# Performance work log

Measured on AMD Instinct MI355X. Metric: run time of the kernel, lower is better.

The kernel has to match this reference:

```python
import jax, jax.numpy as jnp
import numpy as np

EPS = 1e-5

def setup_inputs() -> dict:
    key = jax.random.key(0)
    ks = jax.random.split(key, 4)
    B, N, L, D, H = 1, 32, 512, 256, 8
    msa = jax.random.normal(ks[0], (B, N, L, D), dtype=jnp.float32)
    pair_bias = jax.random.normal(ks[1], (B, L, L, H), dtype=jnp.float32)
    # parameters (fan-in scaled like nn.Linear init magnitude)
    w_qkv = jax.random.normal(ks[2], (D, 3 * D), dtype=jnp.float32) / np.sqrt(D)
    b_qkv = jnp.zeros((3 * D,), dtype=jnp.float32)
    w_proj = jax.random.normal(ks[3], (D, D), dtype=jnp.float32) / np.sqrt(D)
    b_proj = jnp.zeros((D,), dtype=jnp.float32)
    ln_w = jnp.ones((D,), dtype=jnp.float32)
    ln_b = jnp.zeros((D,), dtype=jnp.float32)
    return {"msa": msa, "pair_bias": pair_bias, "ln_w": ln_w, "ln_b": ln_b,
            "w_qkv": w_qkv, "b_qkv": b_qkv, "w_proj": w_proj, "b_proj": b_proj}

def reference(msa, pair_bias, ln_w, ln_b, w_qkv, b_qkv, w_proj, b_proj):
    B, N, L, D = msa.shape
    H = pair_bias.shape[-1]
    hd = D // H
    # LayerNorm over last dim (biased variance, eps=1e-5, as in nn.LayerNorm)
    mu = jnp.mean(msa, axis=-1, keepdims=True)
    var = jnp.mean(jnp.square(msa - mu), axis=-1, keepdims=True)
    m = (msa - mu) * jax.lax.rsqrt(var + EPS) * ln_w + ln_b
    # fused QKV projection; output dim 3*D splits as (3, H, hd)
    qkv = jnp.einsum('bnld,de->bnle', m, w_qkv) + b_qkv  # (B,N,L,3D)
    qkv = qkv.reshape(B, N, L, 3, H, hd)
    q = qkv[:, :, :, 0]  # (B,N,L,H,hd)
    k = qkv[:, :, :, 1]
    v = qkv[:, :, :, 2]
    scale = 1.0 / np.sqrt(hd).astype(np.float32)
    attn = jnp.einsum('bnqhd,bnkhd->bnhqk', q, k) * scale  # (B,N,H,L,L)
    # pair bias (B,L,L,H) -> (B,1,H,L,L), broadcast over the N_seq rows
    attn = attn + jnp.transpose(pair_bias, (0, 3, 1, 2))[:, None]
    attn = jax.nn.softmax(attn, axis=-1)
    out = jnp.einsum('bnhqk,bnkhd->bnqhd', attn, v).reshape(B, N, L, D)
    out = jnp.einsum('bnld,de->bnle', out, w_proj) + b_proj
    return msa + out
```

## Files before the change

kernel.cpp:

```cpp
#include <hip/hip_runtime.h>
#include <hip/hip_bf16.h>

typedef __attribute__((ext_vector_type(8))) short short8;
typedef __attribute__((ext_vector_type(4))) float f32x4;

#define LOG2E 1.4426950408889634f
#define QSCALE 0.25505403955318165f

static __device__ __forceinline__ unsigned short f2bf(float f){
  union { float f; unsigned u; } v; v.f = f;
  unsigned r = v.u + 0x7fffu + ((v.u >> 16) & 1u);
  return (unsigned short)(r >> 16);
}
static __device__ __forceinline__ float bf2f(unsigned short s){
  union { unsigned u; float f; } v; v.u = ((unsigned)s) << 16; return v.f;
}
static __device__ __forceinline__ unsigned cvt_pk_bf16(float lo, float hi){
  unsigned r;
  asm("v_cvt_pk_bf16_f32 %0, %1, %2" : "=v"(r) : "v"(lo), "v"(hi));
  return r;
}
static __device__ __forceinline__ void gload_lds16(const void* g, void* l){
  __builtin_amdgcn_global_load_lds((const __attribute__((address_space(1))) unsigned*)g,
                                   (__attribute__((address_space(3))) unsigned*)l, 16, 0, 0);
}

__global__ __launch_bounds__(256) void k_prep(
    const float* __restrict__ w_qkv, const float* __restrict__ w_proj,
    const float* __restrict__ pb, const float* __restrict__ msa,
    const float* __restrict__ ln_w, const float* __restrict__ ln_b,
    unsigned short* __restrict__ wqkvT, unsigned short* __restrict__ wprojT,
    unsigned short* __restrict__ bt, unsigned short* __restrict__ m_bf){
  __shared__ float tile[64][65];
  int b = blockIdx.x;
  int tid = threadIdx.x;
  if (b < 64){
    const float* in;
    unsigned short* outp;
    int C, tc;
    if (b < 48){ in = w_qkv; outp = wqkvT; C = 768; tc = 12; b -= 0; }
    else       { in = w_proj; outp = wprojT; C = 256; tc = 4;  b -= 48; }
    int r0 = (b / tc) * 64, c0 = (b % tc) * 64;
#pragma unroll
    for (int it = 0; it < 16; it++){
      int idx = tid + it*256, ri = idx >> 6, ci = idx & 63;
      tile[ri][ci] = in[(size_t)(r0+ri)*C + c0+ci];
    }
    __syncthreads();
#pragma unroll
    for (int it = 0; it < 16; it++){
      int idx = tid + it*256, co = idx >> 6, ro = idx & 63;
      outp[(size_t)(c0+co)*256 + r0+ro] = f2bf(tile[ro][co]);
    }
  } else if (b < 1088){
    int bid = b - 64;
    int q = bid >> 1;
    int k = ((bid & 1) << 8) + tid;
    int kc = k >> 6, tl = (k >> 4) & 3, gg = (k >> 2) & 3, r = k & 3;
    int kp = kc*64 + gg*16 + tl*4 + r;
    const float* src = pb + ((size_t)q * 512 + k) * 8;
    float4 a = *(const float4*)src;
    float4 c = *(const float4*)(src + 4);
    float hv[8] = {a.x, a.y, a.z, a.w, c.x, c.y, c.z, c.w};
#pragma unroll
    for (int hh = 0; hh < 8; hh++)
      bt[((size_t)hh * 512 + q) * 512 + kp] = f2bf(hv[hh] * LOG2E);
  } else {
    int wave = tid >> 6, lane = tid & 63;
    int row = (b - 1088) * 4 + wave;
    const float* xr = msa + (size_t)row * 256 + lane * 4;
    float4 v = *(const float4*)xr;
    float s  = v.x + v.y + v.z + v.w;
    float sq = v.x*v.x + v.y*v.y + v.z*v.z + v.w*v.w;
#pragma unroll
    for (int off = 1; off < 64; off <<= 1){ s += __shfl_xor(s, off); sq += __shfl_xor(sq, off); }
    float mu = s * (1.0f/256.0f);
    float var = sq * (1.0f/256.0f) - mu*mu;
    float rs = rsqrtf(var + 1e-5f);
    float4 wv = *(const float4*)(ln_w + lane*4);
    float4 bv = *(const float4*)(ln_b + lane*4);
    uint2 o;
    o.x = cvt_pk_bf16((v.x-mu)*rs*wv.x + bv.x, (v.y-mu)*rs*wv.y + bv.y);
    o.y = cvt_pk_bf16((v.z-mu)*rs*wv.z + bv.z, (v.w-mu)*rs*wv.w + bv.w);
    *(uint2*)(m_bf + (size_t)row * 256 + lane * 4) = o;
  }
}

__global__ __launch_bounds__(256) void k_gemm_qkv(const unsigned short* __restrict__ A,
    const unsigned short* __restrict__ Bt, const float* __restrict__ bias,
    unsigned short* __restrict__ Qb, unsigned short* __restrict__ Kb, unsigned short* __restrict__ Vb){
  __shared__ unsigned short As[128*64];
  __shared__ unsigned short Bs[128*64];
  int bid0 = blockIdx.x;
  int bid = (bid0 & 7) * 96 + (bid0 >> 3);
  int bn = bid % 6, bm = bid / 6;
  int m0 = bm * 128, e0 = bn * 128;
  int t = threadIdx.x, lane = t & 63, w = t >> 6;
  int wm = w >> 1, wn = w & 1;
  int g = lane >> 4, mm = lane & 15;
  f32x4 acc[4][4] = {};
  for (int k0 = 0; k0 < 256; k0 += 64){
    __syncthreads();
#pragma unroll
    for (int it = 0; it < 4; it++){
      int task = t + it * 256;
      int row = task >> 3, ch = task & 7;
      gload_lds16(A  + (size_t)(m0+row)*256 + k0 + ch*8, &As[task*8]);
      gload_lds16(Bt + (size_t)(e0+row)*256 + k0 + ch*8, &Bs[task*8]);
    }
    __syncthreads();
#pragma unroll
    for (int kst = 0; kst < 2; kst++){
      short8 a[4], bb[4];
#pragma unroll
      for (int i = 0; i < 4; i++)
        a[i]  = *(short8*)(&As[(wm*64 + i*16 + mm)*64 + kst*32 + g*8]);
#pragma unroll
      for (int j = 0; j < 4; j++)
        bb[j] = *(short8*)(&Bs[(wn*64 + j*16 + mm)*64 + kst*32 + g*8]);
#pragma unroll
      for (int i = 0; i < 4; i++)
#pragma unroll
        for (int j = 0; j < 4; j++)
          acc[i][j] = __builtin_amdgcn_mfma_f32_16x16x32_bf16(a[i], bb[j], acc[i][j], 0, 0, 0);
    }
  }
#pragma unroll
  for (int i = 0; i < 4; i++)
#pragma unroll
    for (int j = 0; j < 4; j++){
      int col = e0 + wn*64 + j*16 + mm;
      float bc = bias[col];
      int sidx = col >> 8, hh = (col >> 5) & 7, d = col & 31;
      unsigned short* dst = (sidx == 0) ? Qb : ((sidx == 1) ? Kb : Vb);
      float sc = (sidx == 0) ? QSCALE : 1.0f;
#pragma unroll
      for (int r = 0; r < 4; r++){
        int gm = m0 + wm*64 + i*16 + 4*g + r;
        int nn = gm >> 9, l = gm & 511;
        dst[(((size_t)nn*8 + hh)*512 + l)*32 + d] = f2bf((acc[i][j][r] + bc) * sc);
      }
    }
}

__global__ __launch_bounds__(512) void k_attn(const unsigned short* __restrict__ Qb,
    const unsigned short* __restrict__ Kb, const unsigned short* __restrict__ Vb,
    const unsigned short* __restrict__ bt, unsigned short* __restrict__ Ob){
  __shared__ unsigned short Ks[512*40];
  __shared__ unsigned short Vs[32*520];
  int bid = blockIdx.x;
  int h = bid & 7;
  int n = (bid >> 3) & 31;
  int qq = bid >> 8;
  int nh = n*8 + h;
  int t = threadIdx.x;
  int lane = t & 63, wv = t >> 6;
  int g = lane >> 4, q16 = lane & 15;
  const unsigned short* kbase = Kb + (size_t)nh * 16384;
  const unsigned short* vbase = Vb + (size_t)nh * 16384;
  const unsigned short* qbase = Qb + (size_t)nh * 16384;
  {
    int row = t;
    const uint4* ksrc = (const uint4*)(kbase + row * 32);
#pragma unroll
    for (int j = 0; j < 4; j++) *(uint4*)(&Ks[row*40 + j*8]) = ksrc[j];
    int prow = (row & ~12) | ((row & 4) << 1) | ((row & 8) >> 1);
    const uint* vsrc = (const uint*)(vbase + row * 32);
    uint vv[16];
#pragma unroll
    for (int j = 0; j < 16; j++) vv[j] = vsrc[j];
#pragma unroll
    for (int j = 0; j < 16; j++){
      Vs[(2*j)*520 + prow]   = (unsigned short)(vv[j] & 0xffffu);
      Vs[(2*j+1)*520 + prow] = (unsigned short)(vv[j] >> 16);
    }
  }
  __syncthreads();
  {
    int qb = qq*128 + wv*16;
    int qg = qb + q16;
    short8 qf = *(const short8*)(qbase + (size_t)qg * 32 + g * 8);
    const unsigned short* bq = bt + ((size_t)(h*512 + qg))*512 + g*16;
    f32x4 ls4 = {0.0f, 0.0f, 0.0f, 0.0f};
    f32x4 acc[2] = {{0,0,0,0},{0,0,0,0}};
    f32x4 zf = {0.0f, 0.0f, 0.0f, 0.0f};
    uint4 bn0 = *(const uint4*)(bq);
    uint4 bn1 = *(const uint4*)(bq + 8);
#pragma unroll 2
    for (int kc = 0; kc < 8; kc++){
      union { uint4 w[2]; unsigned short u[16]; } bu;
      bu.w[0] = bn0; bu.w[1] = bn1;
      if (kc < 7){
        bn0 = *(const uint4*)(bq + (kc+1)*64);
        bn1 = *(const uint4*)(bq + (kc+1)*64 + 8);
      }
      f32x4 s[4];
      __builtin_amdgcn_s_setprio(1);
#pragma unroll
      for (int tl = 0; tl < 4; tl++){
        short8 kf = *(short8*)(&Ks[(kc*64 + tl*16 + q16)*40 + g*8]);
        s[tl] = __builtin_amdgcn_mfma_f32_16x16x32_bf16(kf, qf, zf, 0, 0, 0);
      }
      __builtin_amdgcn_s_setprio(0);
#pragma unroll
      for (int tl = 0; tl < 4; tl++){
        f32x4 pz;
#pragma unroll
        for (int r = 0; r < 4; r++){
          float e = __builtin_amdgcn_exp2f(s[tl][r] + bf2f(bu.u[tl*4+r]));
          pz[r] = e;
          ls4[r] += e;
        }
        s[tl] = pz;
      }
#pragma unroll
      for (int cl = 0; cl < 2; cl++){
        unsigned a0 = cvt_pk_bf16(s[2*cl][0],   s[2*cl][1]);
        unsigned a1 = cvt_pk_bf16(s[2*cl][2],   s[2*cl][3]);
        unsigned b0 = cvt_pk_bf16(s[2*cl+1][0], s[2*cl+1][1]);
        unsigned b1 = cvt_pk_bf16(s[2*cl+1][2], s[2*cl+1][3]);
        asm("v_permlane32_swap_b32 %0, %1" : "+v"(a0), "+v"(b0));
        asm("v_permlane32_swap_b32 %0, %1" : "+v"(a1), "+v"(b1));
        union { unsigned w[4]; short8 pf; } u;
        u.w[0] = a0; u.w[1] = a1; u.w[2] = b0; u.w[3] = b1;
        __builtin_amdgcn_s_setprio(1);
#pragma unroll
        for (int half = 0; half < 2; half++){
          short8 vf = *(short8*)(&Vs[(half*16 + q16)*520 + kc*64 + cl*32 + g*8]);
          acc[half] = __builtin_amdgcn_mfma_f32_16x16x32_bf16(u.pf, vf, acc[half], 0, 0, 0);
        }
        __builtin_amdgcn_s_setprio(0);
      }
    }
    float ls = (ls4[0] + ls4[1]) + (ls4[2] + ls4[3]);
    ls += __shfl_xor(ls, 16);
    ls += __shfl_xor(ls, 32);
    float linv[4];
#pragma unroll
    for (int r = 0; r < 4; r++) linv[r] = 1.0f / __shfl(ls, 4*g + r);
#pragma unroll
    for (int half = 0; half < 2; half++)
#pragma unroll
      for (int r = 0; r < 4; r++){
        int ql = qb + 4*g + r;
        Ob[((size_t)n*512 + ql)*256 + h*32 + half*16 + q16] = f2bf(acc[half][r] * linv[r]);
      }
  }
}

__global__ __launch_bounds__(256) void k_gemm_proj(const unsigned short* __restrict__ A,
    const unsigned short* __restrict__ Bt, const float* __restrict__ bias,
    const float* __restrict__ msa, float* __restrict__ out){
  __shared__ unsigned short As[64*64];
  __shared__ unsigned short Bs[128*64];
  int bid0 = blockIdx.x;
  int bid = (bid0 & 7) * 64 + (bid0 >> 3);
  int bn = bid & 1, bm = bid >> 1;
  int m0 = bm * 64, e0 = bn * 128;
  int t = threadIdx.x, lane = t & 63, w = t >> 6;
  int g = lane >> 4, mm = lane & 15;
  f32x4 acc[4][2] = {};
  for (int k0 = 0; k0 < 256; k0 += 64){
    __syncthreads();
#pragma unroll
    for (int it = 0; it < 2; it++){
      int task = t + it * 256;
      gload_lds16(A + (size_t)(m0+(task>>3))*256 + k0 + (task&7)*8, &As[task*8]);
    }
#pragma unroll
    for (int it = 0; it < 4; it++){
      int task = t + it * 256;
      gload_lds16(Bt + (size_t)(e0+(task>>3))*256 + k0 + (task&7)*8, &Bs[task*8]);
    }
    __syncthreads();
#pragma unroll
    for (int kst = 0; kst < 2; kst++){
      short8 a[4], bb[2];
#pragma unroll
      for (int i = 0; i < 4; i++)
        a[i] = *(short8*)(&As[(i*16 + mm)*64 + kst*32 + g*8]);
#pragma unroll
      for (int j = 0; j < 2; j++)
        bb[j] = *(short8*)(&Bs[(w*32 + j*16 + mm)*64 + kst*32 + g*8]);
#pragma unroll
      for (int i = 0; i < 4; i++)
#pragma unroll
        for (int j = 0; j < 2; j++)
          acc[i][j] = __builtin_amdgcn_mfma_f32_16x16x32_bf16(a[i], bb[j], acc[i][j], 0, 0, 0);
    }
  }
#pragma unroll
  for (int i = 0; i < 4; i++)
#pragma unroll
    for (int j = 0; j < 2; j++){
      int col = e0 + w*32 + j*16 + mm;
      float bc = bias[col];
#pragma unroll
      for (int r = 0; r < 4; r++){
        int gm = m0 + i*16 + 4*g + r;
        size_t idx = (size_t)gm * 256 + col;
        out[idx] = acc[i][j][r] + bc + msa[idx];
      }
    }
}

extern "C" void kernel_launch(void* const* d_in, const int* in_sizes, int n_in,
                              void* d_out, int out_size, void* d_ws, size_t ws_size,
                              hipStream_t stream){
  const float* msa    = (const float*)d_in[0];
  const float* pb     = (const float*)d_in[1];
  const float* ln_w   = (const float*)d_in[2];
  const float* ln_b   = (const float*)d_in[3];
  const float* w_qkv  = (const float*)d_in[4];
  const float* b_qkv  = (const float*)d_in[5];
  const float* w_proj = (const float*)d_in[6];
  const float* b_proj = (const float*)d_in[7];

  unsigned short* ws     = (unsigned short*)d_ws;
  unsigned short* m_bf   = ws;
  unsigned short* wqkvT  = m_bf   + 4194304;
  unsigned short* wprojT = wqkvT  + 196608;
  unsigned short* Qb     = wprojT + 65536;
  unsigned short* Kb     = Qb     + 4194304;
  unsigned short* Vb     = Kb     + 4194304;
  unsigned short* Ob     = Vb     + 4194304;
  unsigned short* bt     = Ob     + 4194304;
  float* out = (float*)d_out;

  k_prep<<<5184, 256, 0, stream>>>(w_qkv, w_proj, pb, msa, ln_w, ln_b, wqkvT, wprojT, bt, m_bf);
  k_gemm_qkv<<<768, 256, 0, stream>>>(m_bf, wqkvT, b_qkv, Qb, Kb, Vb);
  k_attn<<<1024, 512, 0, stream>>>(Qb, Kb, Vb, bt, Ob);
  k_gemm_proj<<<512, 256, 0, stream>>>(Ob, wprojT, b_proj, msa, out);
}
```

Baseline: 66.66 us.

## Process two query tiles per attention block to reuse staged K/V

Each attention block now handles 256 query rows (two 16-row tiles per wave) instead of 128, halving the grid to 512 blocks. The K and V tiles staged in LDS, including the transposed V copy, are reused across twice as many queries, which halves the global K/V loading and staging work. Two independent MFMA chains per wave also add instruction-level parallelism. In exchange, register pressure roughly doubles and there are fewer blocks, which may reduce occupancy and the ability to hide latency across the 256 CUs.

After: 65.69 us. About the same (-1.4%).

```diff
diff --git a/kernel.cpp b/kernel.cpp
--- a/kernel.cpp
+++ b/kernel.cpp
@@ -151,7 +151,7 @@
   int bid = blockIdx.x;
   int h = bid & 7;
   int n = (bid >> 3) & 31;
-  int qq = bid >> 8;
+  int qh = bid >> 8;
   int nh = n*8 + h;
   int t = threadIdx.x;
   int lane = t & 63, wv = t >> 6;
@@ -177,73 +177,94 @@
   }
   __syncthreads();
   {
-    int qb = qq*128 + wv*16;
-    int qg = qb + q16;
-    short8 qf = *(const short8*)(qbase + (size_t)qg * 32 + g * 8);
-    const unsigned short* bq = bt + ((size_t)(h*512 + qg))*512 + g*16;
-    f32x4 ls4 = {0.0f, 0.0f, 0.0f, 0.0f};
-    f32x4 acc[2] = {{0,0,0,0},{0,0,0,0}};
+    int qb = qh*256 + wv*16;
+    int qgA = qb + q16, qgB = qgA + 128;
+    short8 qfA = *(const short8*)(qbase + (size_t)qgA * 32 + g * 8);
+    short8 qfB = *(const short8*)(qbase + (size_t)qgB * 32 + g * 8);
+    const unsigned short* bqA = bt + ((size_t)(h*512 + qgA))*512 + g*16;
+    const unsigned short* bqB = bt + ((size_t)(h*512 + qgB))*512 + g*16;
+    f32x4 lsA = {0.0f, 0.0f, 0.0f, 0.0f}, lsB = {0.0f, 0.0f, 0.0f, 0.0f};
+    f32x4 accA[2] = {{0,0,0,0},{0,0,0,0}};
+    f32x4 accB[2] = {{0,0,0,0},{0,0,0,0}};
     f32x4 zf = {0.0f, 0.0f, 0.0f, 0.0f};
-    uint4 bn0 = *(const uint4*)(bq);
-    uint4 bn1 = *(const uint4*)(bq + 8);
+    uint4 bnA0 = *(const uint4*)(bqA), bnA1 = *(const uint4*)(bqA + 8);
+    uint4 bnB0 = *(const uint4*)(bqB), bnB1 = *(const uint4*)(bqB + 8);
 #pragma unroll 2
     for (int kc = 0; kc < 8; kc++){
-      union { uint4 w[2]; unsigned short u[16]; } bu;
-      bu.w[0] = bn0; bu.w[1] = bn1;
+      union { uint4 w[2]; unsigned short u[16]; } buA, buB;
+      buA.w[0] = bnA0; buA.w[1] = bnA1;
+      buB.w[0] = bnB0; buB.w[1] = bnB1;
       if (kc < 7){
-        bn0 = *(const uint4*)(bq + (kc+1)*64);
-        bn1 = *(const uint4*)(bq + (kc+1)*64 + 8);
-      }
-      f32x4 s[4];
+        bnA0 = *(const uint4*)(bqA + (kc+1)*64);
+        bnA1 = *(const uint4*)(bqA + (kc+1)*64 + 8);
+        bnB0 = *(const uint4*)(bqB + (kc+1)*64);
+        bnB1 = *(const uint4*)(bqB + (kc+1)*64 + 8);
+      }
+      f32x4 sA[4], sB[4];
       __builtin_amdgcn_s_setprio(1);
 #pragma unroll
       for (int tl = 0; tl < 4; tl++){
         short8 kf = *(short8*)(&Ks[(kc*64 + tl*16 + q16)*40 + g*8]);
-        s[tl] = __builtin_amdgcn_mfma_f32_16x16x32_bf16(kf, qf, zf, 0, 0, 0);
+        sA[tl] = __builtin_amdgcn_mfma_f32_16x16x32_bf16(kf, qfA, zf, 0, 0, 0);
+        sB[tl] = __builtin_amdgcn_mfma_f32_16x16x32_bf16(kf, qfB, zf, 0, 0, 0);
       }
       __builtin_amdgcn_s_setprio(0);
 #pragma unroll
       for (int tl = 0; tl < 4; tl++){
-        f32x4 pz;
 #pragma unroll
         for (int r = 0; r < 4; r++){
-          float e = __builtin_amdgcn_exp2f(s[tl][r] + bf2f(bu.u[tl*4+r]));
-          pz[r] = e;
-          ls4[r] += e;
+          float eA = __builtin_amdgcn_exp2f(sA[tl][r] + bf2f(buA.u[tl*4+r]));
+          sA[tl][r] = eA; lsA[r] += eA;
+          float eB = __builtin_amdgcn_exp2f(sB[tl][r] + bf2f(buB.u[tl*4+r]));
+          sB[tl][r] = eB; lsB[r] += eB;
         }
-        s[tl] = pz;
       }
 #pragma unroll
       for (int cl = 0; cl < 2; cl++){
-        unsigned a0 = cvt_pk_bf16(s[2*cl][0],   s[2*cl][1]);
-        unsigned a1 = cvt_pk_bf16(s[2*cl][2],   s[2*cl][3]);
-        unsigned b0 = cvt_pk_bf16(s[2*cl+1][0], s[2*cl+1][1]);
-        unsigned b1 = cvt_pk_bf16(s[2*cl+1][2], s[2*cl+1][3]);
-        asm("v_permlane32_swap_b32 %0, %1" : "+v"(a0), "+v"(b0));
-        asm("v_permlane32_swap_b32 %0, %1" : "+v"(a1), "+v"(b1));
-        union { unsigned w[4]; short8 pf; } u;
-        u.w[0] = a0; u.w[1] = a1; u.w[2] = b0; u.w[3] = b1;
+        unsigned a0A = cvt_pk_bf16(sA[2*cl][0],   sA[2*cl][1]);
+        unsigned a1A = cvt_pk_bf16(sA[2*cl][2],   sA[2*cl][3]);
+        unsigned b0A = cvt_pk_bf16(sA[2*cl+1][0], sA[2*cl+1][1]);
+        unsigned b1A = cvt_pk_bf16(sA[2*cl+1][2], sA[2*cl+1][3]);
+        asm("v_permlane32_swap_b32 %0, %1" : "+v"(a0A), "+v"(b0A));
+        asm("v_permlane32_swap_b32 %0, %1" : "+v"(a1A), "+v"(b1A));
+        unsigned a0B = cvt_pk_bf16(sB[2*cl][0],   sB[2*cl][1]);
+        unsigned a1B = cvt_pk_bf16(sB[2*cl][2],   sB[2*cl][3]);
+        unsigned b0B = cvt_pk_bf16(sB[2*cl+1][0], sB[2*cl+1][1]);
+        unsigned b1B = cvt_pk_bf16(sB[2*cl+1][2], sB[2*cl+1][3]);
+        asm("v_permlane32_swap_b32 %0, %1" : "+v"(a0B), "+v"(b0B));
+        asm("v_permlane32_swap_b32 %0, %1" : "+v"(a1B), "+v"(b1B));
+        union { unsigned w[4]; short8 pf; } uA, uB;
+        uA.w[0] = a0A; uA.w[1] = a1A; uA.w[2] = b0A; uA.w[3] = b1A;
+        uB.w[0] = a0B; uB.w[1] = a1B; uB.w[2] = b0B; uB.w[3] = b1B;
         __builtin_amdgcn_s_setprio(1);
 #pragma unroll
         for (int half = 0; half < 2; half++){
           short8 vf = *(short8*)(&Vs[(half*16 + q16)*520 + kc*64 + cl*32 + g*8]);
-          acc[half] = __builtin_amdgcn_mfma_f32_16x16x32_bf16(u.pf, vf, acc[half], 0, 0, 0);
+          accA[half] = __builtin_amdgcn_mfma_f32_16x16x32_bf16(uA.pf, vf, accA[half], 0, 0, 0);
+          accB[half] = __builtin_amdgcn_mfma_f32_16x16x32_bf16(uB.pf, vf, accB[half], 0, 0, 0);
         }
         __builtin_amdgcn_s_setprio(0);
       }
     }
-    float ls = (ls4[0] + ls4[1]) + (ls4[2] + ls4[3]);
-    ls += __shfl_xor(ls, 16);
-    ls += __shfl_xor(ls, 32);
-    float linv[4];
-#pragma unroll
-    for (int r = 0; r < 4; r++) linv[r] = 1.0f / __shfl(ls, 4*g + r);
+    float lA = (lsA[0] + lsA[1]) + (lsA[2] + lsA[3]);
+    lA += __shfl_xor(lA, 16);
+    lA += __shfl_xor(lA, 32);
+    float lB = (lsB[0] + lsB[1]) + (lsB[2] + lsB[3]);
+    lB += __shfl_xor(lB, 16);
+    lB += __shfl_xor(lB, 32);
+    float linvA[4], linvB[4];
+#pragma unroll
+    for (int r = 0; r < 4; r++){
+      linvA[r] = 1.0f / __shfl(lA, 4*g + r);
+      linvB[r] = 1.0f / __shfl(lB, 4*g + r);
+    }
 #pragma unroll
     for (int half = 0; half < 2; half++)
 #pragma unroll
       for (int r = 0; r < 4; r++){
         int ql = qb + 4*g + r;
-        Ob[((size_t)n*512 + ql)*256 + h*32 + half*16 + q16] = f2bf(acc[half][r] * linv[r]);
+        Ob[((size_t)n*512 + ql)*256 + h*32 + half*16 + q16] = f2bf(accA[half][r] * linvA[r]);
+        Ob[((size_t)n*512 + ql + 128)*256 + h*32 + half*16 + q16] = f2bf(accB[half][r] * linvB[r]);
       }
   }
 }
@@ -329,6 +350,6 @@
 
   k_prep<<<5184, 256, 0, stream>>>(w_qkv, w_proj, pb, msa, ln_w, ln_b, wqkvT, wprojT, bt, m_bf);
   k_gemm_qkv<<<768, 256, 0, stream>>>(m_bf, wqkvT, b_qkv, Qb, Kb, Vb);
-  k_attn<<<1024, 512, 0, stream>>>(Qb, Kb, Vb, bt, Ob);
+  k_attn<<<512, 512, 0, stream>>>(Qb, Kb, Vb, bt, Ob);
   k_gemm_proj<<<512, 256, 0, stream>>>(Ob, wprojT, b_proj, msa, out);
 }
```

## Stage K/V in two halves to halve attention LDS footprint

Applied to the files above, without the earlier changes.

The attention kernel now stages K and V into shared memory 256 keys at a time instead of all 512, with threads 0-255 loading K and 256-511 loading V. Shared memory per block roughly halves, which could let more blocks reside per CU. The cost is an extra pair of barriers mid-loop plus a serialized reload that is not overlapped with compute. Each thread also does half as much staging work, with a different split of threads between the K and V loads.

Result: slower. 69.77 us (+4.7%).

```diff
diff --git a/kernel.cpp b/kernel.cpp
--- a/kernel.cpp
+++ b/kernel.cpp
@@ -146,8 +146,8 @@
 __global__ __launch_bounds__(512) void k_attn(const unsigned short* __restrict__ Qb,
     const unsigned short* __restrict__ Kb, const unsigned short* __restrict__ Vb,
     const unsigned short* __restrict__ bt, unsigned short* __restrict__ Ob){
-  __shared__ unsigned short Ks[512*40];
-  __shared__ unsigned short Vs[32*520];
+  __shared__ unsigned short Ks[256*40];
+  __shared__ unsigned short Vs[32*260];
   int bid = blockIdx.x;
   int h = bid & 7;
   int n = (bid >> 3) & 31;
@@ -159,35 +159,51 @@
   const unsigned short* kbase = Kb + (size_t)nh * 16384;
   const unsigned short* vbase = Vb + (size_t)nh * 16384;
   const unsigned short* qbase = Qb + (size_t)nh * 16384;
-  {
-    int row = t;
-    const uint4* ksrc = (const uint4*)(kbase + row * 32);
-#pragma unroll
-    for (int j = 0; j < 4; j++) *(uint4*)(&Ks[row*40 + j*8]) = ksrc[j];
-    int prow = (row & ~12) | ((row & 4) << 1) | ((row & 8) >> 1);
-    const uint* vsrc = (const uint*)(vbase + row * 32);
-    uint vv[16];
-#pragma unroll
-    for (int j = 0; j < 16; j++) vv[j] = vsrc[j];
-#pragma unroll
-    for (int j = 0; j < 16; j++){
-      Vs[(2*j)*520 + prow]   = (unsigned short)(vv[j] & 0xffffu);
-      Vs[(2*j+1)*520 + prow] = (unsigned short)(vv[j] >> 16);
-    }
-  }
+
+  auto stage_half = [&](int hf){
+    if (t < 256){
+      int row = hf*256 + t;
+      const uint4* ksrc = (const uint4*)(kbase + (size_t)row * 32);
+#pragma unroll
+      for (int j = 0; j < 4; j++) *(uint4*)(&Ks[t*40 + j*8]) = ksrc[j];
+    } else {
+      int tt = t - 256;
+      int row = hf*256 + tt;
+      int prow = (tt & ~12) | ((tt & 4) << 1) | ((tt & 8) >> 1);
+      const uint* vsrc = (const uint*)(vbase + (size_t)row * 32);
+      uint vv[16];
+#pragma unroll
+      for (int j = 0; j < 16; j++) vv[j] = vsrc[j];
+#pragma unroll
+      for (int j = 0; j < 16; j++){
+        Vs[(2*j)*260 + prow]   = (unsigned short)(vv[j] & 0xffffu);
+        Vs[(2*j+1)*260 + prow] = (unsigned short)(vv[j] >> 16);
+      }
+    }
+  };
+
+  int qb = qq*128 + wv*16;
+  int qg = qb + q16;
+  short8 qf = *(const short8*)(qbase + (size_t)qg * 32 + g * 8);
+  const unsigned short* bq = bt + ((size_t)(h*512 + qg))*512 + g*16;
+  f32x4 ls4 = {0.0f, 0.0f, 0.0f, 0.0f};
+  f32x4 acc[2] = {{0,0,0,0},{0,0,0,0}};
+  f32x4 zf = {0.0f, 0.0f, 0.0f, 0.0f};
+  uint4 bn0 = *(const uint4*)(bq);
+  uint4 bn1 = *(const uint4*)(bq + 8);
+
+  stage_half(0);
   __syncthreads();
-  {
-    int qb = qq*128 + wv*16;
-    int qg = qb + q16;
-    short8 qf = *(const short8*)(qbase + (size_t)qg * 32 + g * 8);
-    const unsigned short* bq = bt + ((size_t)(h*512 + qg))*512 + g*16;
-    f32x4 ls4 = {0.0f, 0.0f, 0.0f, 0.0f};
-    f32x4 acc[2] = {{0,0,0,0},{0,0,0,0}};
-    f32x4 zf = {0.0f, 0.0f, 0.0f, 0.0f};
-    uint4 bn0 = *(const uint4*)(bq);
-    uint4 bn1 = *(const uint4*)(bq + 8);
+#pragma unroll
+  for (int hf = 0; hf < 2; hf++){
+    if (hf == 1){
+      __syncthreads();
+      stage_half(1);
+      __syncthreads();
+    }
 #pragma unroll 2
-    for (int kc = 0; kc < 8; kc++){
+    for (int kcl = 0; kcl < 4; kcl++){
+      int kc = hf*4 + kcl;
       union { uint4 w[2]; unsigned short u[16]; } bu;
       bu.w[0] = bn0; bu.w[1] = bn1;
       if (kc < 7){
@@ -198,7 +214,7 @@
       __builtin_amdgcn_s_setprio(1);
 #pragma unroll
       for (int tl = 0; tl < 4; tl++){
-        short8 kf = *(short8*)(&Ks[(kc*64 + tl*16 + q16)*40 + g*8]);
+        short8 kf = *(short8*)(&Ks[(kcl*64 + tl*16 + q16)*40 + g*8]);
         s[tl] = __builtin_amdgcn_mfma_f32_16x16x32_bf16(kf, qf, zf, 0, 0, 0);
       }
       __builtin_amdgcn_s_setprio(0);
@@ -226,26 +242,26 @@
         __builtin_amdgcn_s_setprio(1);
 #pragma unroll
         for (int half = 0; half < 2; half++){
-          short8 vf = *(short8*)(&Vs[(half*16 + q16)*520 + kc*64 + cl*32 + g*8]);
+          short8 vf = *(short8*)(&Vs[(half*16 + q16)*260 + kcl*64 + cl*32 + g*8]);
           acc[half] = __builtin_amdgcn_mfma_f32_16x16x32_bf16(u.pf, vf, acc[half], 0, 0, 0);
         }
         __builtin_amdgcn_s_setprio(0);
       }
     }
-    float ls = (ls4[0] + ls4[1]) + (ls4[2] + ls4[3]);
-    ls += __shfl_xor(ls, 16);
-    ls += __shfl_xor(ls, 32);
-    float linv[4];
-#pragma unroll
-    for (int r = 0; r < 4; r++) linv[r] = 1.0f / __shfl(ls, 4*g + r);
-#pragma unroll
-    for (int half = 0; half < 2; half++)
-#pragma unroll
-      for (int r = 0; r < 4; r++){
-        int ql = qb + 4*g + r;
-        Ob[((size_t)n*512 + ql)*256 + h*32 + half*16 + q16] = f2bf(acc[half][r] * linv[r]);
-      }
   }
+  float ls = (ls4[0] + ls4[1]) + (ls4[2] + ls4[3]);
+  ls += __shfl_xor(ls, 16);
+  ls += __shfl_xor(ls, 32);
+  float linv[4];
+#pragma unroll
+  for (int r = 0; r < 4; r++) linv[r] = 1.0f / __shfl(ls, 4*g + r);
+#pragma unroll
+  for (int half = 0; half < 2; half++)
+#pragma unroll
+    for (int r = 0; r < 4; r++){
+      int ql = qb + 4*g + r;
+      Ob[((size_t)n*512 + ql)*256 + h*32 + half*16 + q16] = f2bf(acc[half][r] * linv[r]);
+    }
 }
 
 __global__ __launch_bounds__(256) void k_gemm_proj(const unsigned short* __restrict__ A,
```

## Software-pipeline QK MFMA ahead of softmax/PV and pack V transpose stores

Applied to the files above, without the earlier changes.

The attention loop is restructured so the QK^T MFMAs for the next key chunk are issued before the exp/PV work of the current chunk, using ping-pong score buffers, so matrix and vector work can overlap. The V transpose into LDS now has each thread take a pair of rows and write packed 32-bit words instead of single 16-bit stores, which halves the LDS store count. In exchange, the extra score buffers raise register pressure and may lower occupancy.

Result: slower. 68.81 us (+3.2%).

```diff
diff --git a/kernel.cpp b/kernel.cpp
--- a/kernel.cpp
+++ b/kernel.cpp
@@ -164,15 +164,22 @@
     const uint4* ksrc = (const uint4*)(kbase + row * 32);
 #pragma unroll
     for (int j = 0; j < 4; j++) *(uint4*)(&Ks[row*40 + j*8]) = ksrc[j];
-    int prow = (row & ~12) | ((row & 4) << 1) | ((row & 8) >> 1);
-    const uint* vsrc = (const uint*)(vbase + row * 32);
-    uint vv[16];
-#pragma unroll
-    for (int j = 0; j < 16; j++) vv[j] = vsrc[j];
-#pragma unroll
-    for (int j = 0; j < 16; j++){
-      Vs[(2*j)*520 + prow]   = (unsigned short)(vv[j] & 0xffffu);
-      Vs[(2*j+1)*520 + prow] = (unsigned short)(vv[j] >> 16);
+    int p2 = t >> 1, hf = t & 1;
+    int r0 = p2 * 2;
+    int prow0 = (r0 & ~12) | ((r0 & 4) << 1) | ((r0 & 8) >> 1);
+    const uint4* v0 = (const uint4*)(vbase + (size_t)r0*32 + hf*16);
+    const uint4* v1 = (const uint4*)(vbase + (size_t)(r0+1)*32 + hf*16);
+    uint4 a0 = v0[0], a1 = v0[1];
+    uint4 b0 = v1[0], b1 = v1[1];
+    unsigned ua[8] = {a0.x,a0.y,a0.z,a0.w,a1.x,a1.y,a1.z,a1.w};
+    unsigned ub[8] = {b0.x,b0.y,b0.z,b0.w,b1.x,b1.y,b1.z,b1.w};
+#pragma unroll
+    for (int j = 0; j < 8; j++){
+      int d0 = hf*16 + 2*j;
+      unsigned lo = (ua[j] & 0xffffu) | (ub[j] << 16);
+      unsigned hi = (ua[j] >> 16) | (ub[j] & 0xffff0000u);
+      *(unsigned*)(&Vs[d0*520 + prow0])     = lo;
+      *(unsigned*)(&Vs[(d0+1)*520 + prow0]) = hi;
     }
   }
   __syncthreads();
@@ -184,17 +191,8 @@
     f32x4 ls4 = {0.0f, 0.0f, 0.0f, 0.0f};
     f32x4 acc[2] = {{0,0,0,0},{0,0,0,0}};
     f32x4 zf = {0.0f, 0.0f, 0.0f, 0.0f};
-    uint4 bn0 = *(const uint4*)(bq);
-    uint4 bn1 = *(const uint4*)(bq + 8);
-#pragma unroll 2
-    for (int kc = 0; kc < 8; kc++){
-      union { uint4 w[2]; unsigned short u[16]; } bu;
-      bu.w[0] = bn0; bu.w[1] = bn1;
-      if (kc < 7){
-        bn0 = *(const uint4*)(bq + (kc+1)*64);
-        bn1 = *(const uint4*)(bq + (kc+1)*64 + 8);
-      }
-      f32x4 s[4];
+
+    auto qk = [&](int kc, f32x4* s){
       __builtin_amdgcn_s_setprio(1);
 #pragma unroll
       for (int tl = 0; tl < 4; tl++){
@@ -202,6 +200,10 @@
         s[tl] = __builtin_amdgcn_mfma_f32_16x16x32_bf16(kf, qf, zf, 0, 0, 0);
       }
       __builtin_amdgcn_s_setprio(0);
+    };
+    auto process = [&](int kc, f32x4* s, uint4 w0, uint4 w1){
+      union { uint4 w[2]; unsigned short u[16]; } bu;
+      bu.w[0] = w0; bu.w[1] = w1;
 #pragma unroll
       for (int tl = 0; tl < 4; tl++){
         f32x4 pz;
@@ -231,7 +233,27 @@
         }
         __builtin_amdgcn_s_setprio(0);
       }
-    }
+    };
+
+    f32x4 sE[4], sO[4];
+    uint4 c0 = *(const uint4*)(bq);
+    uint4 c1 = *(const uint4*)(bq + 8);
+    qk(0, sE);
+#pragma unroll
+    for (int pp = 0; pp < 4; pp++){
+      int kcE = 2*pp, kcO = 2*pp + 1;
+      uint4 n0 = *(const uint4*)(bq + kcO*64);
+      uint4 n1 = *(const uint4*)(bq + kcO*64 + 8);
+      qk(kcO, sO);
+      process(kcE, sE, c0, c1);
+      if (pp < 3){
+        c0 = *(const uint4*)(bq + (kcE+2)*64);
+        c1 = *(const uint4*)(bq + (kcE+2)*64 + 8);
+        qk(kcE+2, sE);
+      }
+      process(kcO, sO, n0, n1);
+    }
+
     float ls = (ls4[0] + ls4[1]) + (ls4[2] + ls4[3]);
     ls += __shfl_xor(ls, 16);
     ls += __shfl_xor(ls, 32);
```
